# Kernel tuning notes

Measured on AMD Instinct MI355X. Metric: run time of the kernel, lower is better.

Reference implementation:

```python
import jax, jax.numpy as jnp
import numpy as np

B, S, DX, DH = 8, 4096, 1024, 1024

def setup_inputs() -> dict:
    key = jax.random.key(0)
    ks = jax.random.split(key, 7)
    s_x = 1.0 / np.sqrt(DX)
    s_h = 1.0 / np.sqrt(DH)
    return {
        "x":  jax.random.normal(ks[0], (B, S, DX), dtype=jnp.float32),
        "Wz": jax.random.uniform(ks[1], (DH, DX), jnp.float32, -s_x, s_x),
        "bz": jax.random.uniform(ks[2], (DH,),   jnp.float32, -s_x, s_x),
        "Wh": jax.random.uniform(ks[3], (DH, DX), jnp.float32, -s_x, s_x),
        "bh": jax.random.uniform(ks[4], (DH,),   jnp.float32, -s_x, s_x),
        "Wo": jax.random.uniform(ks[5], (DX, DH), jnp.float32, -s_h, s_h),
        "bo": jax.random.uniform(ks[6], (DX,),   jnp.float32, -s_h, s_h),
    }

def log_g(x):
    # Appendix B.3 of "Were RNNs All We Needed?"
    return jnp.where(x >= 0, jnp.log(jax.nn.relu(x) + 0.5), -jax.nn.softplus(-x))

def parallel_scan_log(log_coeffs, log_values):
    # Heinsen log-space associative scan: h_t = a_t * h_{t-1} + b_t (h_0 = 0)
    a_star = jnp.cumsum(log_coeffs, axis=1)                       # [B,S,H]
    log_h = a_star + jax.lax.cumlogsumexp(log_values - a_star, axis=1)
    return jnp.exp(log_h)

def reference(x, Wz, bz, Wh, bh, Wo, bo):
    k       = jnp.einsum('bsd,hd->bsh', x, Wz) + bz               # pre-gate
    tilde_h = jnp.einsum('bsd,hd->bsh', x, Wh) + bh               # candidate
    log_z           = -jax.nn.softplus(-k)                        # log sigmoid(k)
    log_one_minus_z = -jax.nn.softplus(k)                         # log sigmoid(-k)
    log_tilde_h     = log_g(tilde_h)
    h = parallel_scan_log(log_one_minus_z, log_z + log_tilde_h)   # [B,S,H]
    out = jnp.einsum('bsh,dh->bsd', h, Wo) + bo                   # [B,S,DX]
    return out
```

## Files before the change

kernel.cpp:

```cpp
#include <hip/hip_runtime.h>
#include <stdint.h>
#include <stddef.h>


typedef __bf16 bf16;
typedef __bf16 bf16x8 __attribute__((ext_vector_type(8)));
typedef float f32x4 __attribute__((ext_vector_type(4)));

#define DEV __device__ __forceinline__

DEV void gload_lds16(const bf16* g, bf16* l) {
  __builtin_amdgcn_global_load_lds((const __attribute__((address_space(1))) void*)g,
                                   (__attribute__((address_space(3))) void*)l,
                                   16, 0, 0);
}

__global__ __launch_bounds__(256)
void conv_b(const float* __restrict__ src, bf16* __restrict__ dst, int n4) {
  const int stride = gridDim.x * 256;
  for (int i = blockIdx.x * 256 + threadIdx.x; i < n4; i += stride) {
    float4 v = ((const float4*)src)[i];
    bf16 o[4] = {(bf16)v.x, (bf16)v.y, (bf16)v.z, (bf16)v.w};
    *(uint64_t*)(dst + 4 * (size_t)i) = *(uint64_t*)o;
  }
}

__global__ __launch_bounds__(256)
void conv_w3(const float* __restrict__ s0, const float* __restrict__ s1,
             const float* __restrict__ s2,
             bf16* __restrict__ d0, bf16* __restrict__ d1, bf16* __restrict__ d2) {
  const int stride = gridDim.x * 256;
  for (int i = blockIdx.x * 256 + threadIdx.x; i < 786432; i += stride) {
    const float* s; bf16* d; int off;
    if (i < 262144)      { s = s0; d = d0; off = i; }
    else if (i < 524288) { s = s1; d = d1; off = i - 262144; }
    else                 { s = s2; d = d2; off = i - 524288; }
    float4 v = ((const float4*)s)[off];
    bf16 o[4] = {(bf16)v.x, (bf16)v.y, (bf16)v.z, (bf16)v.w};
    *(uint64_t*)(d + 4 * (size_t)off) = *(uint64_t*)o;
  }
}

DEV void xcd_tiles(int bx, int by, int& tileM, int& tileN) {
  const int d = by * 8 + bx;
  const int xcd = d & 7;
  const int i = d >> 3;
  tileM = (xcd * 32 + (i >> 3)) * 128;
  tileN = (i & 7) * 128;
}

__global__ __launch_bounds__(256, 2)
void gate_gemm(const bf16* __restrict__ X,
               const bf16* __restrict__ Wz, const bf16* __restrict__ Wh,
               const float* __restrict__ bzf, const float* __restrict__ bhf,
               bf16* __restrict__ aB, bf16* __restrict__ vB) {
  __shared__ __align__(16) bf16 As [2 * 4096];
  __shared__ __align__(16) bf16 Bzs[2 * 4096];
  __shared__ __align__(16) bf16 Bhs[2 * 4096];

  const int lane = threadIdx.x & 63;
  const int wave = threadIdx.x >> 6;
  const int wm = wave >> 1, wn = wave & 1;
  int tileM, tileN;
  xcd_tiles(blockIdx.x, blockIdx.y, tileM, tileN);
  const int q = lane >> 4, r = lane & 15;
  const int srow = lane >> 2;
  const int scol = (lane & 3) * 8;

  const bf16* ga[2]; const bf16* gz[2]; const bf16* gh[2];
  bf16* la[2]; bf16* lz[2]; bf16* lh[2];
#pragma unroll
  for (int j = 0; j < 2; ++j) {
    const int cid = j * 4 + wave;
    const int row = cid * 16 + srow;
    ga[j] = X  + (size_t)(tileM + row) * 1024 + scol;
    gz[j] = Wz + (size_t)(tileN + row) * 1024 + scol;
    gh[j] = Wh + (size_t)(tileN + row) * 1024 + scol;
    la[j] = As  + cid * 512;
    lz[j] = Bzs + cid * 512;
    lh[j] = Bhs + cid * 512;
  }

  const bf16* pA[4]; const bf16* pBz[4]; const bf16* pBh[4];
#pragma unroll
  for (int f = 0; f < 4; ++f) {
    pA[f]  = As  + (wm * 64 + f * 16 + r) * 32 + q * 8;
    pBz[f] = Bzs + (wn * 64 + f * 16 + r) * 32 + q * 8;
    pBh[f] = Bhs + (wn * 64 + f * 16 + r) * 32 + q * 8;
  }

  f32x4 accz[4][4], acch[4][4];
#pragma unroll
  for (int i = 0; i < 4; ++i)
#pragma unroll
    for (int j = 0; j < 4; ++j) {
      accz[i][j] = (f32x4){0.f, 0.f, 0.f, 0.f};
      acch[i][j] = (f32x4){0.f, 0.f, 0.f, 0.f};
    }

  auto STAGE = [&](int buf, int k0) {
    const int bo = buf * 4096;
#pragma unroll
    for (int j = 0; j < 2; ++j) {
      gload_lds16(ga[j] + k0, la[j] + bo);
      gload_lds16(gz[j] + k0, lz[j] + bo);
      gload_lds16(gh[j] + k0, lh[j] + bo);
    }
  };
  auto COMPUTE = [&](int buf) {
    const int bo = buf * 4096;
    bf16x8 af[4];
#pragma unroll
    for (int fm = 0; fm < 4; ++fm) af[fm] = *(const bf16x8*)(pA[fm] + bo);
#pragma unroll
    for (int fn = 0; fn < 4; ++fn) {
      bf16x8 bz8 = *(const bf16x8*)(pBz[fn] + bo);
      bf16x8 bh8 = *(const bf16x8*)(pBh[fn] + bo);
#pragma unroll
      for (int fm = 0; fm < 4; ++fm) {
        accz[fm][fn] = __builtin_amdgcn_mfma_f32_16x16x32_bf16(af[fm], bz8, accz[fm][fn], 0, 0, 0);
        acch[fm][fn] = __builtin_amdgcn_mfma_f32_16x16x32_bf16(af[fm], bh8, acch[fm][fn], 0, 0, 0);
      }
    }
  };

  STAGE(0, 0);
  int cur = 0;
  for (int t = 0; t < 31; ++t) {
    __syncthreads();
    STAGE(cur ^ 1, (t + 1) * 32);
    COMPUTE(cur);
    cur ^= 1;
  }
  __syncthreads();
  COMPUTE(cur);

#pragma unroll
  for (int fn = 0; fn < 4; ++fn) {
    const int n = tileN + wn * 64 + fn * 16 + r;
    const float bzv = bzf[n], bhv = bhf[n];
#pragma unroll
    for (int fm = 0; fm < 4; ++fm) {
      const int m0 = tileM + wm * 64 + fm * 16 + q * 4;
#pragma unroll
      for (int i = 0; i < 4; ++i) {
        float kv = accz[fm][fn][i] + bzv;
        float tv = acch[fm][fn][i] + bhv;
        float e   = __expf(-kv);
        float inv = 1.f / (1.f + e);
        float a   = e * inv;
        float g   = (tv >= 0.f) ? (tv + 0.5f) : (1.f / (1.f + __expf(-tv)));
        size_t idx = (size_t)(m0 + i) * 1024 + n;
        aB[idx] = (bf16)a;
        vB[idx] = (bf16)(inv * g);
      }
    }
  }
}

__global__ __launch_bounds__(256)
void chk_gate(const bf16* __restrict__ X,
              const bf16* __restrict__ Wz, const bf16* __restrict__ Wh,
              const float* __restrict__ bzf, const float* __restrict__ bhf,
              const bf16* __restrict__ aB, const bf16* __restrict__ vB,
              int* __restrict__ badA) {
  const int w = (blockIdx.x * 256 + threadIdx.x) >> 6;
  const int lane = threadIdx.x & 63;
  const int m = (w * 12347) & 32767;
  const int n = (w * 4099) & 1023;
  float kz = 0.f, kh = 0.f;
  for (int k = lane; k < 1024; k += 64) {
    float xv = (float)X[(size_t)m * 1024 + k];
    kz = fmaf(xv, (float)Wz[(size_t)n * 1024 + k], kz);
    kh = fmaf(xv, (float)Wh[(size_t)n * 1024 + k], kh);
  }
#pragma unroll
  for (int off = 32; off; off >>= 1) {
    kz += __shfl_xor(kz, off);
    kh += __shfl_xor(kh, off);
  }
  if (lane == 0) {
    kz += bzf[n]; kh += bhf[n];
    float e = __expf(-kz), inv = 1.f / (1.f + e);
    float a = e * inv;
    float g = (kh >= 0.f) ? (kh + 0.5f) : (1.f / (1.f + __expf(-kh)));
    float v = inv * g;
    size_t idx = (size_t)m * 1024 + n;
    int ok = (fabsf((float)aB[idx] - a) <= 0.04f) &&
             (fabsf((float)vB[idx] - v) <= 0.08f);
    if (!ok) atomicAdd(badA, 1);
  }
}

__global__ __launch_bounds__(256)
void fb_gate(const int* __restrict__ badA, const bf16* __restrict__ X,
             const bf16* __restrict__ Wz, const bf16* __restrict__ Wh,
             const float* __restrict__ bzf, const float* __restrict__ bhf,
             bf16* __restrict__ aB, bf16* __restrict__ vB) {
  if (*badA < 4) return;
  const int n = (blockIdx.x & 3) * 256 + threadIdx.x;
  const int m0 = (blockIdx.x >> 2) * 16;
  for (int mi = 0; mi < 16; ++mi) {
    const int m = m0 + mi;
    float kz = 0.f, kh = 0.f;
    for (int k = 0; k < 1024; ++k) {
      float xv = (float)X[(size_t)m * 1024 + k];
      kz = fmaf(xv, (float)Wz[(size_t)n * 1024 + k], kz);
      kh = fmaf(xv, (float)Wh[(size_t)n * 1024 + k], kh);
    }
    kz += bzf[n]; kh += bhf[n];
    float e = __expf(-kz), inv = 1.f / (1.f + e);
    float a = e * inv;
    float g = (kh >= 0.f) ? (kh + 0.5f) : (1.f / (1.f + __expf(-kh)));
    size_t idx = (size_t)m * 1024 + n;
    aB[idx] = (bf16)a;
    vB[idx] = (bf16)(inv * g);
  }
}

__global__ __launch_bounds__(256)
void scan_phase1(const bf16* __restrict__ aB, const bf16* __restrict__ vB,
                 float* __restrict__ Ac, float* __restrict__ Vc) {
  const int tid = blockIdx.x * 256 + threadIdx.x;
  const int hg = tid & 127, c = (tid >> 7) & 63, b = tid >> 13;
  const size_t base = (size_t)(b * 4096 + c * 64) * 1024 + hg * 8;
  float A[8], V[8];
#pragma unroll
  for (int j = 0; j < 8; ++j) { A[j] = 1.f; V[j] = 0.f; }
#pragma unroll 8
  for (int t = 0; t < 64; ++t) {
    bf16x8 a8 = *(const bf16x8*)(aB + base + (size_t)t * 1024);
    bf16x8 v8 = *(const bf16x8*)(vB + base + (size_t)t * 1024);
#pragma unroll
    for (int j = 0; j < 8; ++j) {
      float a = (float)a8[j];
      V[j] = fmaf(a, V[j], (float)v8[j]);
      A[j] *= a;
    }
  }
  const size_t o = (size_t)(b * 64 + c) * 1024 + hg * 8;
#pragma unroll
  for (int j = 0; j < 8; ++j) { Ac[o + j] = A[j]; Vc[o + j] = V[j]; }
}

__global__ __launch_bounds__(256)
void scan_phase2(const float* __restrict__ Ac, const float* __restrict__ Vc,
                 float* __restrict__ Hin) {
  const int tid = blockIdx.x * 256 + threadIdx.x;
  const int h = tid & 1023, b = tid >> 10;
  float carry = 0.f;
  for (int c = 0; c < 64; ++c) {
    const int idx = (b * 64 + c) * 1024 + h;
    Hin[idx] = carry;
    carry = fmaf(Ac[idx], carry, Vc[idx]);
  }
}

__global__ __launch_bounds__(256)
void scan_phase3(const bf16* __restrict__ aB, const bf16* vB,
                 const float* __restrict__ Hin, bf16* hB) {
  const int tid = blockIdx.x * 256 + threadIdx.x;
  const int hg = tid & 127, c = (tid >> 7) & 63, b = tid >> 13;
  const size_t base = (size_t)(b * 4096 + c * 64) * 1024 + hg * 8;
  const size_t o = (size_t)(b * 64 + c) * 1024 + hg * 8;
  float hc[8];
#pragma unroll
  for (int j = 0; j < 8; ++j) hc[j] = Hin[o + j];
#pragma unroll 4
  for (int t = 0; t < 64; ++t) {
    bf16x8 a8 = *(const bf16x8*)(aB + base + (size_t)t * 1024);
    bf16x8 v8 = *(const bf16x8*)(vB + base + (size_t)t * 1024);
    bf16x8 h8;
#pragma unroll
    for (int j = 0; j < 8; ++j) {
      hc[j] = fmaf((float)a8[j], hc[j], (float)v8[j]);
      h8[j] = (bf16)hc[j];
    }
    *(bf16x8*)(hB + base + (size_t)t * 1024) = h8;
  }
}

__global__ __launch_bounds__(256, 2)
void out_gemm(const bf16* __restrict__ H, const bf16* __restrict__ Wo,
              const float* __restrict__ bof, float* __restrict__ O) {
  __shared__ __align__(16) bf16 As[2 * 4096];
  __shared__ __align__(16) bf16 Bs[2 * 4096];

  const int lane = threadIdx.x & 63;
  const int wave = threadIdx.x >> 6;
  const int wm = wave >> 1, wn = wave & 1;
  int tileM, tileN;
  xcd_tiles(blockIdx.x, blockIdx.y, tileM, tileN);
  const int q = lane >> 4, r = lane & 15;
  const int srow = lane >> 2;
  const int scol = (lane & 3) * 8;

  const bf16* ga[2]; const bf16* gb[2]; bf16* la[2]; bf16* lb[2];
#pragma unroll
  for (int j = 0; j < 2; ++j) {
    const int cid = j * 4 + wave;
    const int row = cid * 16 + srow;
    ga[j] = H  + (size_t)(tileM + row) * 1024 + scol;
    gb[j] = Wo + (size_t)(tileN + row) * 1024 + scol;
    la[j] = As + cid * 512;
    lb[j] = Bs + cid * 512;
  }
  const bf16* pA[4]; const bf16* pB[4];
#pragma unroll
  for (int f = 0; f < 4; ++f) {
    pA[f] = As + (wm * 64 + f * 16 + r) * 32 + q * 8;
    pB[f] = Bs + (wn * 64 + f * 16 + r) * 32 + q * 8;
  }

  f32x4 acc[4][4];
#pragma unroll
  for (int i = 0; i < 4; ++i)
#pragma unroll
    for (int j = 0; j < 4; ++j) acc[i][j] = (f32x4){0.f, 0.f, 0.f, 0.f};

  auto STAGE = [&](int buf, int k0) {
    const int bo = buf * 4096;
#pragma unroll
    for (int j = 0; j < 2; ++j) {
      gload_lds16(ga[j] + k0, la[j] + bo);
      gload_lds16(gb[j] + k0, lb[j] + bo);
    }
  };
  auto COMPUTE = [&](int buf) {
    const int bo = buf * 4096;
    bf16x8 af[4];
#pragma unroll
    for (int fm = 0; fm < 4; ++fm) af[fm] = *(const bf16x8*)(pA[fm] + bo);
#pragma unroll
    for (int fn = 0; fn < 4; ++fn) {
      bf16x8 b8 = *(const bf16x8*)(pB[fn] + bo);
#pragma unroll
      for (int fm = 0; fm < 4; ++fm)
        acc[fm][fn] = __builtin_amdgcn_mfma_f32_16x16x32_bf16(af[fm], b8, acc[fm][fn], 0, 0, 0);
    }
  };

  STAGE(0, 0);
  int cur = 0;
  for (int t = 0; t < 31; ++t) {
    __syncthreads();
    STAGE(cur ^ 1, (t + 1) * 32);
    COMPUTE(cur);
    cur ^= 1;
  }
  __syncthreads();
  COMPUTE(cur);

#pragma unroll
  for (int fn = 0; fn < 4; ++fn) {
    const int n = tileN + wn * 64 + fn * 16 + r;
    const float bov = bof[n];
#pragma unroll
    for (int fm = 0; fm < 4; ++fm) {
      const int m0 = tileM + wm * 64 + fm * 16 + q * 4;
#pragma unroll
      for (int i = 0; i < 4; ++i)
        O[(size_t)(m0 + i) * 1024 + n] = acc[fm][fn][i] + bov;
    }
  }
}

__global__ __launch_bounds__(256)
void chk_out(const bf16* __restrict__ H, const bf16* __restrict__ Wo,
             const float* __restrict__ bof, const float* __restrict__ O,
             int* __restrict__ badB) {
  const int w = (blockIdx.x * 256 + threadIdx.x) >> 6;
  const int lane = threadIdx.x & 63;
  const int m = (w * 12347) & 32767;
  const int n = (w * 4099) & 1023;
  float acc = 0.f;
  for (int k = lane; k < 1024; k += 64)
    acc = fmaf((float)H[(size_t)m * 1024 + k], (float)Wo[(size_t)n * 1024 + k], acc);
#pragma unroll
  for (int off = 32; off; off >>= 1) acc += __shfl_xor(acc, off);
  if (lane == 0) {
    acc += bof[n];
    int ok = fabsf(O[(size_t)m * 1024 + n] - acc) <= 0.05f;
    if (!ok) atomicAdd(badB, 1);
  }
}

__global__ __launch_bounds__(256)
void fb_out(const int* __restrict__ badB, const bf16* __restrict__ H,
            const bf16* __restrict__ Wo, const float* __restrict__ bof,
            float* __restrict__ O) {
  if (*badB < 4) return;
  const int n = (blockIdx.x & 3) * 256 + threadIdx.x;
  const int m0 = (blockIdx.x >> 2) * 16;
  for (int mi = 0; mi < 16; ++mi) {
    const int m = m0 + mi;
    float acc = 0.f;
    for (int k = 0; k < 1024; ++k)
      acc = fmaf((float)H[(size_t)m * 1024 + k], (float)Wo[(size_t)n * 1024 + k], acc);
    O[(size_t)m * 1024 + n] = acc + bof[n];
  }
}

extern "C" void kernel_launch(void* const* d_in, const int* in_sizes, int n_in,
                              void* d_out, int out_size, void* d_ws, size_t ws_size,
                              hipStream_t stream) {
  char* ws = (char*)d_ws;
  bf16*  aB  = (bf16*)(ws);
  bf16*  vB  = (bf16*)(ws + 67108864ull);
  float* Ac  = (float*)(ws + 134217728ull);
  float* Vc  = (float*)(ws + 136314880ull);
  float* Hin = (float*)(ws + 138412032ull);
  int*   flags = (int*)(ws + 140509184ull);
  bf16*  wzb = (bf16*)(ws + 140525568ull);
  bf16*  whb = wzb + 1048576;
  bf16*  wob = whb + 1048576;
  bf16*  xb  = (bf16*)(ws + 148914176ull);

  const float* bzf = (const float*)d_in[2];
  const float* bhf = (const float*)d_in[4];
  const float* bof = (const float*)d_in[6];

  hipMemsetAsync(flags, 0, 8, stream);
  conv_b<<<4096, 256, 0, stream>>>((const float*)d_in[0], xb, 8388608);
  conv_w3<<<3072, 256, 0, stream>>>((const float*)d_in[1], (const float*)d_in[3],
                                    (const float*)d_in[5], wzb, whb, wob);

  dim3 blk(256);
  dim3 gg(8, 256);

  gate_gemm<<<gg, blk, 0, stream>>>(xb, wzb, whb, bzf, bhf, aB, vB);
  chk_gate<<<256, blk, 0, stream>>>(xb, wzb, whb, bzf, bhf, aB, vB, flags);
  fb_gate<<<8192, blk, 0, stream>>>(flags, xb, wzb, whb, bzf, bhf, aB, vB);

  scan_phase1<<<256, blk, 0, stream>>>(aB, vB, Ac, Vc);
  scan_phase2<<<32,  blk, 0, stream>>>(Ac, Vc, Hin);
  scan_phase3<<<256, blk, 0, stream>>>(aB, vB, Hin, vB );

  out_gemm<<<gg, blk, 0, stream>>>(vB, wob, bof, (float*)d_out);
  chk_out<<<256, blk, 0, stream>>>(vB, wob, bof, (const float*)d_out, flags + 1);
  fb_out<<<8192, blk, 0, stream>>>(flags + 1, vB, wob, bof, (float*)d_out);
}
```

Measured before the change: 620.6 us.

## Interleave Wz/Wh rows into one weight matrix and store gates as interleaved pairs

Wz and Wh are packed into a single interleaved [2048,1024] bf16 matrix, so the gate GEMM becomes one standard GEMM with a 16x256 grid. Each shuffle pair of lanes then holds k and tilde-h for the same column. Gate outputs are written as interleaved (a, v) pairs through an LDS-staged, vectorised 16-byte store instead of scattered 2-byte stores. The scan kernels read the interleaved pairs and write h into the reused x buffer. Occupancy hints rise to 3 blocks per CU, and the checker and fallback kernels now validate against the fp32 inputs with extra edge samples.

Result: faster. 605.3 us (-2.5%).

```diff
diff --git a/kernel.cpp b/kernel.cpp
--- a/kernel.cpp
+++ b/kernel.cpp
@@ -13,6 +13,20 @@
   __builtin_amdgcn_global_load_lds((const __attribute__((address_space(1))) void*)g,
                                    (__attribute__((address_space(3))) void*)l,
                                    16, 0, 0);
+}
+
+DEV void xcd_tiles(int bx, int by, int gx_lg, int& tileM, int& tileN) {
+  const int d = (by << gx_lg) + bx;
+  const int xcd = d & 7;
+  const int i = d >> 3;
+  tileM = (xcd * 32 + (i >> gx_lg)) * 128;
+  tileN = (i & ((1 << gx_lg) - 1)) * 128;
+}
+
+DEV void chk_sample(int w, int& m, int& n) {
+  if (w < 64)       { m = w;              n = (w * 97) & 1023; }
+  else if (w < 128) { m = 32767 - (w - 64); n = (w * 97) & 1023; }
+  else              { m = (w * 12347) & 32767; n = (w * 4099) & 1023; }
 }
 
 __global__ __launch_bounds__(256)
@@ -26,85 +40,76 @@
 }
 
 __global__ __launch_bounds__(256)
-void conv_w3(const float* __restrict__ s0, const float* __restrict__ s1,
-             const float* __restrict__ s2,
-             bf16* __restrict__ d0, bf16* __restrict__ d1, bf16* __restrict__ d2) {
+void conv_w3(const float* __restrict__ wz, const float* __restrict__ wh,
+             const float* __restrict__ wo,
+             bf16* __restrict__ w2, bf16* __restrict__ wob) {
   const int stride = gridDim.x * 256;
   for (int i = blockIdx.x * 256 + threadIdx.x; i < 786432; i += stride) {
-    const float* s; bf16* d; int off;
-    if (i < 262144)      { s = s0; d = d0; off = i; }
-    else if (i < 524288) { s = s1; d = d1; off = i - 262144; }
-    else                 { s = s2; d = d2; off = i - 524288; }
-    float4 v = ((const float4*)s)[off];
-    bf16 o[4] = {(bf16)v.x, (bf16)v.y, (bf16)v.z, (bf16)v.w};
-    *(uint64_t*)(d + 4 * (size_t)off) = *(uint64_t*)o;
-  }
-}
-
-DEV void xcd_tiles(int bx, int by, int& tileM, int& tileN) {
-  const int d = by * 8 + bx;
-  const int xcd = d & 7;
-  const int i = d >> 3;
-  tileM = (xcd * 32 + (i >> 3)) * 128;
-  tileN = (i & 7) * 128;
-}
-
-__global__ __launch_bounds__(256, 2)
-void gate_gemm(const bf16* __restrict__ X,
-               const bf16* __restrict__ Wz, const bf16* __restrict__ Wh,
+    if (i < 262144) {
+      const int j = i, n = j >> 8, c = j & 255;
+      float4 v = ((const float4*)wz)[j];
+      bf16 o[4] = {(bf16)v.x, (bf16)v.y, (bf16)v.z, (bf16)v.w};
+      *(uint64_t*)(w2 + 4 * ((size_t)(n << 9) + c)) = *(uint64_t*)o;
+    } else if (i < 524288) {
+      const int j = i - 262144, n = j >> 8, c = j & 255;
+      float4 v = ((const float4*)wh)[j];
+      bf16 o[4] = {(bf16)v.x, (bf16)v.y, (bf16)v.z, (bf16)v.w};
+      *(uint64_t*)(w2 + 4 * ((size_t)(n << 9) + 256 + c)) = *(uint64_t*)o;
+    } else {
+      const int j = i - 524288;
+      float4 v = ((const float4*)wo)[j];
+      bf16 o[4] = {(bf16)v.x, (bf16)v.y, (bf16)v.z, (bf16)v.w};
+      *(uint64_t*)(wob + 4 * (size_t)j) = *(uint64_t*)o;
+    }
+  }
+}
+
+__global__ __launch_bounds__(256, 3)
+void gate_gemm(const bf16* __restrict__ X, const bf16* __restrict__ W2,
                const float* __restrict__ bzf, const float* __restrict__ bhf,
-               bf16* __restrict__ aB, bf16* __restrict__ vB) {
-  __shared__ __align__(16) bf16 As [2 * 4096];
-  __shared__ __align__(16) bf16 Bzs[2 * 4096];
-  __shared__ __align__(16) bf16 Bhs[2 * 4096];
+               bf16* __restrict__ avB) {
+  __shared__ __align__(16) bf16 SMEM[17408];
+  bf16* As = SMEM;
+  bf16* Bs = SMEM + 8192;
 
   const int lane = threadIdx.x & 63;
   const int wave = threadIdx.x >> 6;
   const int wm = wave >> 1, wn = wave & 1;
   int tileM, tileN;
-  xcd_tiles(blockIdx.x, blockIdx.y, tileM, tileN);
+  xcd_tiles(blockIdx.x, blockIdx.y, 4, tileM, tileN);
   const int q = lane >> 4, r = lane & 15;
   const int srow = lane >> 2;
   const int scol = (lane & 3) * 8;
 
-  const bf16* ga[2]; const bf16* gz[2]; const bf16* gh[2];
-  bf16* la[2]; bf16* lz[2]; bf16* lh[2];
+  const bf16* ga[2]; const bf16* gb[2]; bf16* la[2]; bf16* lb[2];
 #pragma unroll
   for (int j = 0; j < 2; ++j) {
     const int cid = j * 4 + wave;
     const int row = cid * 16 + srow;
     ga[j] = X  + (size_t)(tileM + row) * 1024 + scol;
-    gz[j] = Wz + (size_t)(tileN + row) * 1024 + scol;
-    gh[j] = Wh + (size_t)(tileN + row) * 1024 + scol;
-    la[j] = As  + cid * 512;
-    lz[j] = Bzs + cid * 512;
-    lh[j] = Bhs + cid * 512;
-  }
-
-  const bf16* pA[4]; const bf16* pBz[4]; const bf16* pBh[4];
+    gb[j] = W2 + (size_t)(tileN + row) * 1024 + scol;
+    la[j] = As + cid * 512;
+    lb[j] = Bs + cid * 512;
+  }
+  const bf16* pA[4]; const bf16* pB[4];
 #pragma unroll
   for (int f = 0; f < 4; ++f) {
-    pA[f]  = As  + (wm * 64 + f * 16 + r) * 32 + q * 8;
-    pBz[f] = Bzs + (wn * 64 + f * 16 + r) * 32 + q * 8;
-    pBh[f] = Bhs + (wn * 64 + f * 16 + r) * 32 + q * 8;
-  }
-
-  f32x4 accz[4][4], acch[4][4];
+    pA[f] = As + (wm * 64 + f * 16 + r) * 32 + q * 8;
+    pB[f] = Bs + (wn * 64 + f * 16 + r) * 32 + q * 8;
+  }
+
+  f32x4 acc[4][4];
 #pragma unroll
   for (int i = 0; i < 4; ++i)
 #pragma unroll
-    for (int j = 0; j < 4; ++j) {
-      accz[i][j] = (f32x4){0.f, 0.f, 0.f, 0.f};
-      acch[i][j] = (f32x4){0.f, 0.f, 0.f, 0.f};
-    }
+    for (int j = 0; j < 4; ++j) acc[i][j] = (f32x4){0.f, 0.f, 0.f, 0.f};
 
   auto STAGE = [&](int buf, int k0) {
     const int bo = buf * 4096;
 #pragma unroll
     for (int j = 0; j < 2; ++j) {
       gload_lds16(ga[j] + k0, la[j] + bo);
-      gload_lds16(gz[j] + k0, lz[j] + bo);
-      gload_lds16(gh[j] + k0, lh[j] + bo);
+      gload_lds16(gb[j] + k0, lb[j] + bo);
     }
   };
   auto COMPUTE = [&](int buf) {
@@ -114,13 +119,10 @@
     for (int fm = 0; fm < 4; ++fm) af[fm] = *(const bf16x8*)(pA[fm] + bo);
 #pragma unroll
     for (int fn = 0; fn < 4; ++fn) {
-      bf16x8 bz8 = *(const bf16x8*)(pBz[fn] + bo);
-      bf16x8 bh8 = *(const bf16x8*)(pBh[fn] + bo);
-#pragma unroll
-      for (int fm = 0; fm < 4; ++fm) {
-        accz[fm][fn] = __builtin_amdgcn_mfma_f32_16x16x32_bf16(af[fm], bz8, accz[fm][fn], 0, 0, 0);
-        acch[fm][fn] = __builtin_amdgcn_mfma_f32_16x16x32_bf16(af[fm], bh8, acch[fm][fn], 0, 0, 0);
-      }
+      bf16x8 b8 = *(const bf16x8*)(pB[fn] + bo);
+#pragma unroll
+      for (int fm = 0; fm < 4; ++fm)
+        acc[fm][fn] = __builtin_amdgcn_mfma_f32_16x16x32_bf16(af[fm], b8, acc[fm][fn], 0, 0, 0);
     }
   };
 
@@ -135,44 +137,59 @@
   __syncthreads();
   COMPUTE(cur);
 
+  __syncthreads();
+  bf16* C = SMEM;
 #pragma unroll
   for (int fn = 0; fn < 4; ++fn) {
-    const int n = tileN + wn * 64 + fn * 16 + r;
-    const float bzv = bzf[n], bhv = bhf[n];
+    const int cl = wn * 64 + fn * 16 + r;
+    const int n = (tileN + cl) >> 1;
+    const float bz = bzf[n], bh = bhf[n];
 #pragma unroll
     for (int fm = 0; fm < 4; ++fm) {
-      const int m0 = tileM + wm * 64 + fm * 16 + q * 4;
+      const int ml = wm * 64 + fm * 16 + q * 4;
 #pragma unroll
       for (int i = 0; i < 4; ++i) {
-        float kv = accz[fm][fn][i] + bzv;
-        float tv = acch[fm][fn][i] + bhv;
-        float e   = __expf(-kv);
-        float inv = 1.f / (1.f + e);
-        float a   = e * inv;
-        float g   = (tv >= 0.f) ? (tv + 0.5f) : (1.f / (1.f + __expf(-tv)));
-        size_t idx = (size_t)(m0 + i) * 1024 + n;
-        aB[idx] = (bf16)a;
-        vB[idx] = (bf16)(inv * g);
+        const float val = acc[fm][fn][i];
+        const float oth = __shfl_xor(val, 1);
+        const float kraw  = (lane & 1) ? oth : val;
+        const float thraw = (lane & 1) ? val : oth;
+        const float k  = kraw + bz;
+        const float th = thraw + bh;
+        const float e   = __expf(-k);
+        const float inv = 1.f / (1.f + e);
+        const float a   = e * inv;
+        const float g   = (th >= 0.f) ? (th + 0.5f)
+                                      : (1.f / (1.f + __expf(-th)));
+        const float res = (lane & 1) ? (inv * g) : a;
+        C[(ml + i) * 136 + cl] = (bf16)res;
       }
     }
   }
-}
-
-__global__ __launch_bounds__(256)
-void chk_gate(const bf16* __restrict__ X,
-              const bf16* __restrict__ Wz, const bf16* __restrict__ Wh,
+  __syncthreads();
+  const int tT = threadIdx.x;
+#pragma unroll
+  for (int p = 0; p < 8; ++p) {
+    const int row  = p * 16 + (tT >> 4);
+    const int col8 = (tT & 15) * 8;
+    bf16x8 v8 = *(const bf16x8*)(C + row * 136 + col8);
+    *(bf16x8*)(avB + (size_t)(tileM + row) * 2048 + tileN + col8) = v8;
+  }
+}
+
+__global__ __launch_bounds__(256)
+void chk_gate(const float* __restrict__ Xf,
+              const float* __restrict__ Wzf, const float* __restrict__ Whf,
               const float* __restrict__ bzf, const float* __restrict__ bhf,
-              const bf16* __restrict__ aB, const bf16* __restrict__ vB,
-              int* __restrict__ badA) {
+              const bf16* __restrict__ avB, int* __restrict__ badA) {
   const int w = (blockIdx.x * 256 + threadIdx.x) >> 6;
   const int lane = threadIdx.x & 63;
-  const int m = (w * 12347) & 32767;
-  const int n = (w * 4099) & 1023;
+  int m, n;
+  chk_sample(w, m, n);
   float kz = 0.f, kh = 0.f;
   for (int k = lane; k < 1024; k += 64) {
-    float xv = (float)X[(size_t)m * 1024 + k];
-    kz = fmaf(xv, (float)Wz[(size_t)n * 1024 + k], kz);
-    kh = fmaf(xv, (float)Wh[(size_t)n * 1024 + k], kh);
+    float xv = Xf[(size_t)m * 1024 + k];
+    kz = fmaf(xv, Wzf[(size_t)n * 1024 + k], kz);
+    kh = fmaf(xv, Whf[(size_t)n * 1024 + k], kh);
   }
 #pragma unroll
   for (int off = 32; off; off >>= 1) {
@@ -185,18 +202,18 @@
     float a = e * inv;
     float g = (kh >= 0.f) ? (kh + 0.5f) : (1.f / (1.f + __expf(-kh)));
     float v = inv * g;
-    size_t idx = (size_t)m * 1024 + n;
-    int ok = (fabsf((float)aB[idx] - a) <= 0.04f) &&
-             (fabsf((float)vB[idx] - v) <= 0.08f);
+    size_t idx = (size_t)m * 2048 + 2 * n;
+    int ok = (fabsf((float)avB[idx] - a) <= 0.04f) &&
+             (fabsf((float)avB[idx + 1] - v) <= 0.08f);
     if (!ok) atomicAdd(badA, 1);
   }
 }
 
 __global__ __launch_bounds__(256)
-void fb_gate(const int* __restrict__ badA, const bf16* __restrict__ X,
-             const bf16* __restrict__ Wz, const bf16* __restrict__ Wh,
+void fb_gate(const int* __restrict__ badA, const float* __restrict__ Xf,
+             const float* __restrict__ Wzf, const float* __restrict__ Whf,
              const float* __restrict__ bzf, const float* __restrict__ bhf,
-             bf16* __restrict__ aB, bf16* __restrict__ vB) {
+             bf16* __restrict__ avB) {
   if (*badA < 4) return;
   const int n = (blockIdx.x & 3) * 256 + threadIdx.x;
   const int m0 = (blockIdx.x >> 2) * 16;
@@ -204,37 +221,38 @@
     const int m = m0 + mi;
     float kz = 0.f, kh = 0.f;
     for (int k = 0; k < 1024; ++k) {
-      float xv = (float)X[(size_t)m * 1024 + k];
-      kz = fmaf(xv, (float)Wz[(size_t)n * 1024 + k], kz);
-      kh = fmaf(xv, (float)Wh[(size_t)n * 1024 + k], kh);
+      float xv = Xf[(size_t)m * 1024 + k];
+      kz = fmaf(xv, Wzf[(size_t)n * 1024 + k], kz);
+      kh = fmaf(xv, Whf[(size_t)n * 1024 + k], kh);
     }
     kz += bzf[n]; kh += bhf[n];
     float e = __expf(-kz), inv = 1.f / (1.f + e);
     float a = e * inv;
     float g = (kh >= 0.f) ? (kh + 0.5f) : (1.f / (1.f + __expf(-kh)));
-    size_t idx = (size_t)m * 1024 + n;
-    aB[idx] = (bf16)a;
-    vB[idx] = (bf16)(inv * g);
-  }
-}
-
-__global__ __launch_bounds__(256)
-void scan_phase1(const bf16* __restrict__ aB, const bf16* __restrict__ vB,
+    size_t idx = (size_t)m * 2048 + 2 * n;
+    avB[idx] = (bf16)a;
+    avB[idx + 1] = (bf16)(inv * g);
+  }
+}
+
+__global__ __launch_bounds__(256)
+void scan_phase1(const bf16* __restrict__ avB,
                  float* __restrict__ Ac, float* __restrict__ Vc) {
   const int tid = blockIdx.x * 256 + threadIdx.x;
   const int hg = tid & 127, c = (tid >> 7) & 63, b = tid >> 13;
-  const size_t base = (size_t)(b * 4096 + c * 64) * 1024 + hg * 8;
+  const size_t base = (size_t)(b * 4096 + c * 64) * 2048 + hg * 16;
   float A[8], V[8];
 #pragma unroll
   for (int j = 0; j < 8; ++j) { A[j] = 1.f; V[j] = 0.f; }
 #pragma unroll 8
   for (int t = 0; t < 64; ++t) {
-    bf16x8 a8 = *(const bf16x8*)(aB + base + (size_t)t * 1024);
-    bf16x8 v8 = *(const bf16x8*)(vB + base + (size_t)t * 1024);
+    bf16 arr[16];
+    *(bf16x8*)(arr)     = *(const bf16x8*)(avB + base + (size_t)t * 2048);
+    *(bf16x8*)(arr + 8) = *(const bf16x8*)(avB + base + (size_t)t * 2048 + 8);
 #pragma unroll
     for (int j = 0; j < 8; ++j) {
-      float a = (float)a8[j];
-      V[j] = fmaf(a, V[j], (float)v8[j]);
+      float a = (float)arr[2 * j];
+      V[j] = fmaf(a, V[j], (float)arr[2 * j + 1]);
       A[j] *= a;
     }
   }
@@ -257,30 +275,32 @@
 }
 
 __global__ __launch_bounds__(256)
-void scan_phase3(const bf16* __restrict__ aB, const bf16* vB,
-                 const float* __restrict__ Hin, bf16* hB) {
+void scan_phase3(const bf16* __restrict__ avB, const float* __restrict__ Hin,
+                 bf16* __restrict__ hB) {
   const int tid = blockIdx.x * 256 + threadIdx.x;
   const int hg = tid & 127, c = (tid >> 7) & 63, b = tid >> 13;
-  const size_t base = (size_t)(b * 4096 + c * 64) * 1024 + hg * 8;
+  const size_t base = (size_t)(b * 4096 + c * 64) * 2048 + hg * 16;
+  const size_t bout = (size_t)(b * 4096 + c * 64) * 1024 + hg * 8;
   const size_t o = (size_t)(b * 64 + c) * 1024 + hg * 8;
   float hc[8];
 #pragma unroll
   for (int j = 0; j < 8; ++j) hc[j] = Hin[o + j];
 #pragma unroll 4
   for (int t = 0; t < 64; ++t) {
-    bf16x8 a8 = *(const bf16x8*)(aB + base + (size_t)t * 1024);
-    bf16x8 v8 = *(const bf16x8*)(vB + base + (size_t)t * 1024);
+    bf16 arr[16];
+    *(bf16x8*)(arr)     = *(const bf16x8*)(avB + base + (size_t)t * 2048);
+    *(bf16x8*)(arr + 8) = *(const bf16x8*)(avB + base + (size_t)t * 2048 + 8);
     bf16x8 h8;
 #pragma unroll
     for (int j = 0; j < 8; ++j) {
-      hc[j] = fmaf((float)a8[j], hc[j], (float)v8[j]);
+      hc[j] = fmaf((float)arr[2 * j], hc[j], (float)arr[2 * j + 1]);
       h8[j] = (bf16)hc[j];
     }
-    *(bf16x8*)(hB + base + (size_t)t * 1024) = h8;
-  }
-}
-
-__global__ __launch_bounds__(256, 2)
+    *(bf16x8*)(hB + bout + (size_t)t * 1024) = h8;
+  }
+}
+
+__global__ __launch_bounds__(256, 3)
 void out_gemm(const bf16* __restrict__ H, const bf16* __restrict__ Wo,
               const float* __restrict__ bof, float* __restrict__ O) {
   __shared__ __align__(16) bf16 As[2 * 4096];
@@ -290,7 +310,7 @@
   const int wave = threadIdx.x >> 6;
   const int wm = wave >> 1, wn = wave & 1;
   int tileM, tileN;
-  xcd_tiles(blockIdx.x, blockIdx.y, tileM, tileN);
+  xcd_tiles(blockIdx.x, blockIdx.y, 3, tileM, tileN);
   const int q = lane >> 4, r = lane & 15;
   const int srow = lane >> 2;
   const int scol = (lane & 3) * 8;
@@ -366,16 +386,16 @@
 }
 
 __global__ __launch_bounds__(256)
-void chk_out(const bf16* __restrict__ H, const bf16* __restrict__ Wo,
+void chk_out(const bf16* __restrict__ H, const float* __restrict__ Wof,
              const float* __restrict__ bof, const float* __restrict__ O,
              int* __restrict__ badB) {
   const int w = (blockIdx.x * 256 + threadIdx.x) >> 6;
   const int lane = threadIdx.x & 63;
-  const int m = (w * 12347) & 32767;
-  const int n = (w * 4099) & 1023;
+  int m, n;
+  chk_sample(w, m, n);
   float acc = 0.f;
   for (int k = lane; k < 1024; k += 64)
-    acc = fmaf((float)H[(size_t)m * 1024 + k], (float)Wo[(size_t)n * 1024 + k], acc);
+    acc = fmaf((float)H[(size_t)m * 1024 + k], Wof[(size_t)n * 1024 + k], acc);
 #pragma unroll
   for (int off = 32; off; off >>= 1) acc += __shfl_xor(acc, off);
   if (lane == 0) {
@@ -387,7 +407,7 @@
 
 __global__ __launch_bounds__(256)
 void fb_out(const int* __restrict__ badB, const bf16* __restrict__ H,
-            const bf16* __restrict__ Wo, const float* __restrict__ bof,
+            const float* __restrict__ Wof, const float* __restrict__ bof,
             float* __restrict__ O) {
   if (*badB < 4) return;
   const int n = (blockIdx.x & 3) * 256 + threadIdx.x;
@@ -396,7 +416,7 @@
     const int m = m0 + mi;
     float acc = 0.f;
     for (int k = 0; k < 1024; ++k)
-      acc = fmaf((float)H[(size_t)m * 1024 + k], (float)Wo[(size_t)n * 1024 + k], acc);
+      acc = fmaf((float)H[(size_t)m * 1024 + k], Wof[(size_t)n * 1024 + k], acc);
     O[(size_t)m * 1024 + n] = acc + bof[n];
   }
 }
@@ -405,38 +425,40 @@
                               void* d_out, int out_size, void* d_ws, size_t ws_size,
                               hipStream_t stream) {
   char* ws = (char*)d_ws;
-  bf16*  aB  = (bf16*)(ws);
-  bf16*  vB  = (bf16*)(ws + 67108864ull);
+  bf16*  avB = (bf16*)(ws);
   float* Ac  = (float*)(ws + 134217728ull);
   float* Vc  = (float*)(ws + 136314880ull);
   float* Hin = (float*)(ws + 138412032ull);
   int*   flags = (int*)(ws + 140509184ull);
-  bf16*  wzb = (bf16*)(ws + 140525568ull);
-  bf16*  whb = wzb + 1048576;
-  bf16*  wob = whb + 1048576;
-  bf16*  xb  = (bf16*)(ws + 148914176ull);
-
+  bf16*  w2b = (bf16*)(ws + 140525568ull);
+  bf16*  wob = (bf16*)(ws + 144719872ull);
+  bf16*  xb  = (bf16*)(ws + 146817024ull);
+
+  const float* Xf  = (const float*)d_in[0];
+  const float* Wzf = (const float*)d_in[1];
   const float* bzf = (const float*)d_in[2];
+  const float* Whf = (const float*)d_in[3];
   const float* bhf = (const float*)d_in[4];
+  const float* Wof = (const float*)d_in[5];
   const float* bof = (const float*)d_in[6];
 
   hipMemsetAsync(flags, 0, 8, stream);
-  conv_b<<<4096, 256, 0, stream>>>((const float*)d_in[0], xb, 8388608);
-  conv_w3<<<3072, 256, 0, stream>>>((const float*)d_in[1], (const float*)d_in[3],
-                                    (const float*)d_in[5], wzb, whb, wob);
+  conv_b<<<4096, 256, 0, stream>>>(Xf, xb, 8388608);
+  conv_w3<<<3072, 256, 0, stream>>>(Wzf, Whf, Wof, w2b, wob);
 
   dim3 blk(256);
-  dim3 gg(8, 256);
-
-  gate_gemm<<<gg, blk, 0, stream>>>(xb, wzb, whb, bzf, bhf, aB, vB);
-  chk_gate<<<256, blk, 0, stream>>>(xb, wzb, whb, bzf, bhf, aB, vB, flags);
-  fb_gate<<<8192, blk, 0, stream>>>(flags, xb, wzb, whb, bzf, bhf, aB, vB);
-
-  scan_phase1<<<256, blk, 0, stream>>>(aB, vB, Ac, Vc);
+  dim3 gg(16, 256);
+  dim3 go(8, 256);
+
+  gate_gemm<<<gg, blk, 0, stream>>>(xb, w2b, bzf, bhf, avB);
+  chk_gate<<<256, blk, 0, stream>>>(Xf, Wzf, Whf, bzf, bhf, avB, flags);
+  fb_gate<<<8192, blk, 0, stream>>>(flags, Xf, Wzf, Whf, bzf, bhf, avB);
+
+  scan_phase1<<<256, blk, 0, stream>>>(avB, Ac, Vc);
   scan_phase2<<<32,  blk, 0, stream>>>(Ac, Vc, Hin);
-  scan_phase3<<<256, blk, 0, stream>>>(aB, vB, Hin, vB );
-
-  out_gemm<<<gg, blk, 0, stream>>>(vB, wob, bof, (float*)d_out);
-  chk_out<<<256, blk, 0, stream>>>(vB, wob, bof, (const float*)d_out, flags + 1);
-  fb_out<<<8192, blk, 0, stream>>>(flags + 1, vB, wob, bof, (float*)d_out);
-}
+  scan_phase3<<<256, blk, 0, stream>>>(avB, Hin, xb );
+
+  out_gemm<<<go, blk, 0, stream>>>(xb, wob, bof, (float*)d_out);
+  chk_out<<<256, blk, 0, stream>>>(xb, Wof, bof, (const float*)d_out, flags + 1);
+  fb_out<<<8192, blk, 0, stream>>>(flags + 1, xb, Wof, bof, (float*)d_out);
+}
```
